# Kernel tuning notes

Hardware: AMD Instinct MI355X
Metric: run time of the kernel (lower is better)

## Reference

```python
import jax, jax.numpy as jnp
import numpy as np

N = 100000        # n_nodes (entities)
B = 1024          # batch of users
S = 32            # edge_threshold (sampled edges per node)
M = 64            # adj_matrix neighbors per node
D_IN = 64         # in_channel[0]
HID = 32          # out_channel[0] == in_channel[1]
D_OUT = 64        # out_channel[1]
K_STEP = 2
NUM_SAMPLE = 32
ITEM_LO, ITEM_HI = 0, 39999
SLOPE = 0.01      # leaky_relu default negative slope


def setup_inputs() -> dict:
    key = jax.random.key(0)
    ks = jax.random.split(key, 12)
    sc = lambda *sh: 1.0 / np.sqrt(sh[-1])
    return {
        "entity_embedding": jax.random.normal(ks[0], (N, D_IN), jnp.float32) * 0.1,
        "W1l": jax.random.normal(ks[1], (HID, D_IN), jnp.float32) * sc(HID, D_IN),
        "W1r": jax.random.normal(ks[2], (HID, D_IN), jnp.float32) * sc(HID, D_IN),
        "b1": jnp.zeros((HID,), jnp.float32),
        "W2l": jax.random.normal(ks[3], (D_OUT, HID), jnp.float32) * sc(D_OUT, HID),
        "W2r": jax.random.normal(ks[4], (D_OUT, HID), jnp.float32) * sc(D_OUT, HID),
        "b2": jnp.zeros((D_OUT,), jnp.float32),
        "disc_emb": jax.random.normal(ks[5], (N, D_OUT), jnp.float32) * 0.1,
        "users": jax.random.randint(ks[6], (B,), 0, ITEM_HI + 1, jnp.int32),
        "pos": jax.random.randint(ks[7], (B,), 0, ITEM_HI + 1, jnp.int32),
        "adj_matrix": jax.random.randint(ks[8], (N, M), 0, N, jnp.int32),
        "edge_matrix": jax.random.randint(ks[9], (N, S), 0, N, jnp.int32),
    }


def _leaky(x):
    return jnp.where(x >= 0, x, SLOPE * x)


def _sage(x, src, dst, Wl, Wr, b):
    # PyG SAGEConv: lin_l(mean_{j->i} x_j) + lin_r(x_i)
    sums = jax.ops.segment_sum(x[src], dst, num_segments=N)
    cnt = jax.ops.segment_sum(jnp.ones(src.shape, x.dtype), dst, num_segments=N)
    mean = sums / jnp.maximum(cnt, 1.0)[:, None]
    return mean @ Wl.T + b + x @ Wr.T


def _gcn(x, src, dst, W1l, W1r, b1, W2l, W2r, b2):
    h = _leaky(_sage(x, src, dst, W1l, W1r, b1))   # dropout = identity (eval)
    h = _sage(h, src, dst, W2l, W2r, b2)
    nrm = jnp.sqrt(jnp.sum(h * h, axis=1, keepdims=True))
    return h / jnp.maximum(nrm, 1e-12)             # F.normalize


def _kg_step(gcn, pos_idx, users, adj, explore_flag, step):
    u_e = gcn[users]                               # [B, d]
    pos_e = gcn[pos_idx]                           # [B, d]
    one_hop = adj[pos_idx] if explore_flag == 1 else adj[users]   # [B, M]
    i_e = gcn[one_hop]                             # [B, M, d]
    p = jnp.einsum('bmd,bd->bm', _leaky(pos_e[:, None, :] * i_e), u_e)
    logits = jax.nn.softmax(p, axis=1)
    if step == 1:
        nid = jnp.argmax(logits, axis=1)[:, None]
    else:
        _, nid = jax.lax.top_k(logits, NUM_SAMPLE)
    cand = jnp.take_along_axis(one_hop, nid, axis=1)
    prob = jnp.log(jnp.take_along_axis(logits, nid, axis=1))
    if step == 1:
        return cand[:, 0], prob[:, 0]
    return cand, prob


def _filter_entity(cand, key):
    rnd = jax.random.randint(key, cand.shape, ITEM_LO, ITEM_HI + 1, dtype=cand.dtype)
    bad = (cand > ITEM_HI) | (cand < ITEM_LO)
    return jnp.where(bad, rnd, cand)


def _prune_step(disc_emb, users, pos2, negs, logits):
    # stand-in for discriminator.item_rank (no_grad in original)
    u = jax.lax.stop_gradient(disc_emb[users])
    ranking = jnp.einsum('bd,bjd->bj', u,
                         jax.lax.stop_gradient(disc_emb[pos2] - disc_emb[negs]))
    idx = jnp.argmin(ranking, axis=1)[:, None]
    good_neg = jnp.take_along_axis(negs, idx, axis=1)[:, 0]
    good_logits = jnp.take_along_axis(logits, idx, axis=1)[:, 0]
    return good_neg, good_logits


def reference(entity_embedding, W1l, W1r, b1, W2l, W2r, b2, disc_emb,
              users, pos, adj_matrix, edge_matrix):
    src = jnp.repeat(jnp.arange(N, dtype=jnp.int32), S)   # build_edge node_index
    dst = edge_matrix.reshape(-1)
    gcn = _gcn(entity_embedding, src, dst, W1l, W1r, b1, W2l, W2r, b2)
    fkey = jax.random.key(123)
    neg_list, prob_list = [], []
    p = pos
    for k in range(K_STEP):
        one_hop, one_hop_logits = _kg_step(gcn, p, users, adj_matrix, 1, 1)
        cand, two_logits = _kg_step(gcn, one_hop, users, adj_matrix, 1, 2)
        cand = _filter_entity(cand, jax.random.fold_in(fkey, 2 * k))
        pos2, _ = _kg_step(gcn, p, users, adj_matrix, 2, 2)
        pos2 = _filter_entity(pos2, jax.random.fold_in(fkey, 2 * k + 1))
        good_neg, good_logits = _prune_step(disc_emb, users, pos2, cand, two_logits)
        good_logits = good_logits + one_hop_logits
        neg_list.append(good_neg)
        prob_list.append(good_logits)
        p = good_neg
    return jnp.stack(neg_list), jnp.stack(prob_list)
```

## Files before the change

### kernel.cpp

```cpp
#include <hip/hip_runtime.h>
#include <hip/hip_bf16.h>

#define N_NODES 100000
#define N_EDGES (N_NODES * 32)
#define BATCH   1024
#define SPAN    40000u
#define MULT    7296u
#define FILL_B  (N_EDGES / 256)

#define NB_BKT 391
#define EPB    4096
#define SBLK   782
#define BKT_CAP 8960


__host__ __device__ inline void threefry2x32(unsigned k0, unsigned k1,
                                             unsigned x0, unsigned x1,
                                             unsigned* o0, unsigned* o1)
{
  unsigned ks2 = k0 ^ k1 ^ 0x1BD11BDAu;
  unsigned v0 = x0 + k0, v1 = x1 + k1;
#define RL(x,d) (((x) << (d)) | ((x) >> (32 - (d))))
#define G4(a,b,c,dd) \
  v0 += v1; v1 = RL(v1,a);  v1 ^= v0; \
  v0 += v1; v1 = RL(v1,b);  v1 ^= v0; \
  v0 += v1; v1 = RL(v1,c);  v1 ^= v0; \
  v0 += v1; v1 = RL(v1,dd); v1 ^= v0;
  G4(13,15,26,6)  v0 += k1;  v1 += ks2 + 1u;
  G4(17,29,16,24) v0 += ks2; v1 += k0 + 2u;
  G4(13,15,26,6)  v0 += k0;  v1 += k1 + 3u;
  G4(17,29,16,24) v0 += k1;  v1 += ks2 + 4u;
  G4(13,15,26,6)  v0 += ks2; v1 += k0 + 5u;
#undef G4
#undef RL
  *o0 = v0; *o1 = v1;
}

__device__ __forceinline__ float bcastf(float v, int l)
{
  return __int_as_float(__builtin_amdgcn_readlane(__float_as_int(v), l));
}

__device__ __forceinline__ float fbar(float v)
{
  asm volatile("" : "+v"(v));
  return v;
}


__global__ void k_init_buckets(int* __restrict__ bbase, int* __restrict__ bcur)
{
  int i = blockIdx.x * 256 + threadIdx.x;
  if (i < NB_BKT) { bbase[i] = i * BKT_CAP; bcur[i] = i * BKT_CAP; }
}

__global__ __launch_bounds__(256) void k_bucket_hist(
    const int* __restrict__ edge, int* __restrict__ bhist)
{
  __shared__ int h[NB_BKT];
  for (int i = threadIdx.x; i < NB_BKT; i += 256) h[i] = 0;
  __syncthreads();
  int base = blockIdx.x * EPB;
  int cnt = N_EDGES - base; if (cnt > EPB) cnt = EPB;
  const int4* e4 = (const int4*)(edge + base);
  int nq = cnt >> 2;
  for (int i = threadIdx.x; i < nq; i += 256) {
    int4 v = e4[i];
    atomicAdd(&h[v.x >> 8], 1); atomicAdd(&h[v.y >> 8], 1);
    atomicAdd(&h[v.z >> 8], 1); atomicAdd(&h[v.w >> 8], 1);
  }
  __syncthreads();
  for (int i = threadIdx.x; i < NB_BKT; i += 256)
    if (h[i]) atomicAdd(&bhist[i], h[i]);
}

__global__ void k_scan_buckets(const int* __restrict__ bhist,
                               int* __restrict__ bbase, int* __restrict__ bcur)
{
  __shared__ int s[512];
  int t = threadIdx.x;
  s[t] = (t < NB_BKT) ? bhist[t] : 0;
  __syncthreads();
  for (int o = 1; o < 512; o <<= 1) {
    int u = (t >= o) ? s[t - o] : 0;
    __syncthreads();
    s[t] += u;
    __syncthreads();
  }
  if (t < NB_BKT) {
    int excl = s[t] - bhist[t];
    bbase[t] = excl;
    bcur[t]  = excl;
  }
}

__global__ __launch_bounds__(256) void k_bucket_scatter(
    const int* __restrict__ edge, int* __restrict__ bcur,
    int* __restrict__ pairs)
{
  __shared__ int  h[NB_BKT];
  __shared__ int  lbase[NB_BKT];
  __shared__ int  gbase[NB_BKT];
  __shared__ int  lcur[NB_BKT];
  __shared__ int2 buf[EPB];
  int t = threadIdx.x;
  for (int i = t; i < NB_BKT; i += 256) h[i] = 0;
  __syncthreads();
  int base = blockIdx.x * EPB;
  int cnt = N_EDGES - base; if (cnt > EPB) cnt = EPB;
  const int4* e4 = (const int4*)(edge + base);
  int nq = cnt >> 2;
  for (int i = t; i < nq; i += 256) {
    int4 v = e4[i];
    atomicAdd(&h[v.x >> 8], 1); atomicAdd(&h[v.y >> 8], 1);
    atomicAdd(&h[v.z >> 8], 1); atomicAdd(&h[v.w >> 8], 1);
  }
  __syncthreads();
  if (t < 64) {
    int run = 0;
    for (int c = 0; c < NB_BKT; c += 64) {
      int idx = c + t;
      int v = (idx < NB_BKT) ? h[idx] : 0;
      int orig = v;
      for (int o = 1; o < 64; o <<= 1) {
        int u = __shfl_up(v, o);
        if (t >= o) v += u;
      }
      if (idx < NB_BKT) lbase[idx] = run + v - orig;
      run += __shfl(v, 63);
    }
  }
  __syncthreads();
  for (int i = t; i < NB_BKT; i += 256) lcur[i] = lbase[i];
  __syncthreads();
  for (int i = t; i < nq; i += 256) {
    int4 v = e4[i];
    int eid = base + (i << 2);
    int p;
    p = atomicAdd(&lcur[v.x >> 8], 1); buf[p] = make_int2(v.x, (eid + 0) >> 5);
    p = atomicAdd(&lcur[v.y >> 8], 1); buf[p] = make_int2(v.y, (eid + 1) >> 5);
    p = atomicAdd(&lcur[v.z >> 8], 1); buf[p] = make_int2(v.z, (eid + 2) >> 5);
    p = atomicAdd(&lcur[v.w >> 8], 1); buf[p] = make_int2(v.w, (eid + 3) >> 5);
  }
  __syncthreads();
  for (int i = t; i < NB_BKT; i += 256) {
    int c = lcur[i] - lbase[i];
    gbase[i] = (c > 0) ? atomicAdd(&bcur[i], c) : 0;
  }
  __syncthreads();
  for (int i = t; i < cnt; i += 256) {
    int2 pr = buf[i];
    int b = pr.x >> 8;
    pairs[gbase[b] + (i - lbase[b])] = (pr.y << 8) | (pr.x & 255);
  }
}

__global__ __launch_bounds__(256) void k_bucket_csr(
    const int* __restrict__ bbase, const int* __restrict__ bcur,
    const int* __restrict__ pairs, int* __restrict__ csr,
    int* __restrict__ rowp, int* __restrict__ deg)
{
  __shared__ int nd[256], nb[256], nc[256];
  int b = blockIdx.x, t = threadIdx.x;
  int nb0 = b << 8;
  int ebase = bbase[b];
  int ecnt  = bcur[b] - ebase;
  nd[t] = 0; nc[t] = 0;
  __syncthreads();
  for (int i = t; i < ecnt; i += 256) {
    int pr = pairs[ebase + i];
    atomicAdd(&nd[pr & 255], 1);
  }
  __syncthreads();
  nb[t] = nd[t];
  __syncthreads();
  for (int o = 1; o < 256; o <<= 1) {
    int u = (t >= o) ? nb[t - o] : 0;
    __syncthreads();
    nb[t] += u;
    __syncthreads();
  }
  int excl = nb[t] - nd[t];
  int node = nb0 + t;
  if (node < N_NODES) { rowp[node] = ebase + excl; deg[node] = nd[t]; }
  __syncthreads();
  nb[t] = excl;
  __syncthreads();
  for (int i = t; i < ecnt; i += 256) {
    int pr = pairs[ebase + i];
    int l = pr & 255;
    int p = atomicAdd(&nc[l], 1);
    csr[ebase + nb[l] + p] = pr >> 8;
  }
}

__global__ __launch_bounds__(256) void k_gather_csr(
    const int* __restrict__ rowp, const int* __restrict__ deg,
    const int* __restrict__ csr, const float* __restrict__ src,
    float* __restrict__ out)
{
  int node = blockIdx.x * 8 + (threadIdx.x >> 5);
  int f = threadIdx.x & 31;
  int hb = threadIdx.x & 32;
  int sub = f >> 3;
  int q   = f & 7;
  int start = rowp[node];
  int dg = deg[node];
  const float4* src4 = (const float4*)src;
  float4 a0 = make_float4(0.f, 0.f, 0.f, 0.f);
  float4 a1 = make_float4(0.f, 0.f, 0.f, 0.f);
  for (int b0 = 0; b0 < dg; b0 += 32) {
    int idx = b0 + f;
    int e = (idx < dg) ? csr[start + idx] : -1;
#pragma unroll
    for (int j = 0; j < 8; j += 2) {
      int e0 = __shfl(e, hb + 4 * j + sub);
      int e1 = __shfl(e, hb + 4 * (j + 1) + sub);
      if (e0 >= 0) {
        float4 v = src4[(size_t)e0 * 8 + q];
        a0.x += v.x; a0.y += v.y; a0.z += v.z; a0.w += v.w;
      }
      if (e1 >= 0) {
        float4 v = src4[(size_t)e1 * 8 + q];
        a1.x += v.x; a1.y += v.y; a1.z += v.z; a1.w += v.w;
      }
    }
  }
  a0.x += a1.x; a0.y += a1.y; a0.z += a1.z; a0.w += a1.w;
  a0.x += __shfl_xor(a0.x, 8);  a0.y += __shfl_xor(a0.y, 8);
  a0.z += __shfl_xor(a0.z, 8);  a0.w += __shfl_xor(a0.w, 8);
  a0.x += __shfl_xor(a0.x, 16); a0.y += __shfl_xor(a0.y, 16);
  a0.z += __shfl_xor(a0.z, 16); a0.w += __shfl_xor(a0.w, 16);
  if (sub == 0) ((float4*)out)[(size_t)node * 8 + q] = a0;
}

__global__ __launch_bounds__(256) void k_fill_gemm(
    const int* __restrict__ edge, int* __restrict__ head, int* __restrict__ next,
    int nsub, const float* __restrict__ x, const float* __restrict__ W,
    float* __restrict__ y)
{
  __shared__ float sw[32 * 65];
  if (blockIdx.x < FILL_B) {
    int e = blockIdx.x * 256 + threadIdx.x;
    int d = edge[e];
    int sub = e & (nsub - 1);
    int old = atomicExch(head + sub * N_NODES + d, e);
    next[e] = old;
  } else {
    for (int t = threadIdx.x; t < 2048; t += 256) sw[(t >> 6) * 65 + (t & 63)] = W[t];
    __syncthreads();
    int i = (blockIdx.x - FILL_B) * 8 + (threadIdx.x >> 5);
    int f = threadIdx.x & 31;
    const float* xr = x + (size_t)i * 64;
    const float* wr = sw + f * 65;
    float acc = 0.f;
#pragma unroll
    for (int d = 0; d < 64; ++d) acc += xr[d] * wr[d];
    y[(size_t)i * 32 + f] = acc;
  }
}

template<int NSUB>
__global__ __launch_bounds__(256) void k_gather_ll(
    const int* __restrict__ head, const int* __restrict__ next,
    const float* __restrict__ src, float* __restrict__ out,
    int* __restrict__ deg_out)
{
  int node = blockIdx.x * 8 + (threadIdx.x >> 5);
  int f = threadIdx.x & 31;
  int hb = threadIdx.x & 32;
  int e = (f < NSUB) ? head[f * N_NODES + node] : -1;
  float acc = 0.f;
  int cnt = 0;
  while (true) {
    int es[NSUB];
    bool any = false;
#pragma unroll
    for (int j = 0; j < NSUB; ++j) { es[j] = __shfl(e, hb + j); any |= (es[j] != -1); }
    if (!any) break;
    int en = -1;
    if (f < NSUB && e != -1) en = next[e];
#pragma unroll
    for (int j = 0; j < NSUB; ++j)
      if (es[j] != -1) { acc += src[(size_t)(es[j] >> 5) * 32 + f]; cnt++; }
    e = en;
  }
  out[(size_t)node * 32 + f] = acc;
  if (deg_out != nullptr && f == 0) deg_out[node] = cnt;
}

#define DGB 391

__global__ __launch_bounds__(256, 4) void k_gemm64x32(
    const float* __restrict__ x, const float* __restrict__ W, float* __restrict__ y)
{
  int lane = threadIdx.x & 63;
  int wv = blockIdx.x * 4 + (threadIdx.x >> 6);
  int node = wv * 64 + lane;
  bool ok = node < N_NODES;
  const float4* x4 = (const float4*)(x + (size_t)node * 64);
  const float4* W4 = (const float4*)W;
  float acc[32];
#pragma unroll
  for (int o = 0; o < 32; ++o) acc[o] = 0.f;
#pragma unroll 1
  for (int j = 0; j < 16; ++j) {
    float4 xv = ok ? x4[j] : make_float4(0.f, 0.f, 0.f, 0.f);
#pragma unroll
    for (int o = 0; o < 32; ++o) {
      float4 wv4 = W4[o * 16 + j];
      acc[o] += wv4.x * xv.x;
      acc[o] += wv4.y * xv.y;
      acc[o] += wv4.z * xv.z;
      acc[o] += wv4.w * xv.w;
    }
  }
  if (ok) {
    float4* y4 = (float4*)(y + (size_t)node * 32);
#pragma unroll
    for (int k = 0; k < 8; ++k)
      y4[k] = make_float4(acc[4 * k], acc[4 * k + 1], acc[4 * k + 2], acc[4 * k + 3]);
  }
}

__global__ __launch_bounds__(256) void k_scatter(
    const int* __restrict__ edge, const float* __restrict__ src,
    float* __restrict__ acc, int* __restrict__ cnt)
{
  int e = blockIdx.x * 8 + (threadIdx.x >> 5);
  int f = threadIdx.x & 31;
  int d = edge[e];
  atomicAdd(acc + (size_t)d * 32 + f, src[(size_t)(e >> 5) * 32 + f]);
  if (cnt != nullptr && f == 0) atomicAdd(cnt + d, 1);
}

__global__ __launch_bounds__(256, 4) void k_layer1(
    const float* __restrict__ sum1, const int* __restrict__ cnt,
    const float* __restrict__ x, const float* __restrict__ W1r,
    const float* __restrict__ b1, float* __restrict__ h)
{
  int lane = threadIdx.x & 63;
  int wv = blockIdx.x * 4 + (threadIdx.x >> 6);
  int node = wv * 64 + lane;
  bool ok = node < N_NODES;
  const float4* x4 = (const float4*)(x + (size_t)node * 64);
  const float4* W4 = (const float4*)W1r;
  float acc[32];
#pragma unroll
  for (int o = 0; o < 32; ++o) acc[o] = 0.f;
#pragma unroll 1
  for (int j = 0; j < 16; ++j) {
    float4 xv = ok ? x4[j] : make_float4(0.f, 0.f, 0.f, 0.f);
#pragma unroll
    for (int o = 0; o < 32; ++o) {
      float4 wv4 = W4[o * 16 + j];
      acc[o] += wv4.x * xv.x;
      acc[o] += wv4.y * xv.y;
      acc[o] += wv4.z * xv.z;
      acc[o] += wv4.w * xv.w;
    }
  }
  if (ok) {
    float c = fmaxf((float)cnt[node], 1.f);
    const float4* s4 = (const float4*)(sum1 + (size_t)node * 32);
    float4* h4 = (float4*)(h + (size_t)node * 32);
#pragma unroll
    for (int k = 0; k < 8; ++k) {
      float4 sv = s4[k];
      float4 r;
      r.x = ((sv.x / c) + b1[4 * k + 0]) + acc[4 * k + 0];
      r.y = ((sv.y / c) + b1[4 * k + 1]) + acc[4 * k + 1];
      r.z = ((sv.z / c) + b1[4 * k + 2]) + acc[4 * k + 2];
      r.w = ((sv.w / c) + b1[4 * k + 3]) + acc[4 * k + 3];
      r.x = (r.x >= 0.f) ? r.x : 0.01f * r.x;
      r.y = (r.y >= 0.f) ? r.y : 0.01f * r.y;
      r.z = (r.z >= 0.f) ? r.z : 0.01f * r.z;
      r.w = (r.w >= 0.f) ? r.w : 0.01f * r.w;
      h4[k] = r;
    }
  }
}

#define L2B 782

__global__ __launch_bounds__(256, 4) void k_layer2(
    float* __restrict__ A, float* __restrict__ B, const int* __restrict__ cnt,
    const float* __restrict__ W2l, const float* __restrict__ W2r,
    const float* __restrict__ b2)
{
  int lane = threadIdx.x & 63;
  int wv = blockIdx.x * 4 + (threadIdx.x >> 6);
  int node = wv * 32 + (lane >> 1);
  int half = lane & 1;
  bool ok = node < N_NODES;
  float c = 1.f;
  if (ok) c = fmaxf((float)cnt[node], 1.f);
  const float4* B4 = (const float4*)(B + (size_t)node * 32);
  const float4* A4 = (const float4*)(A + (size_t)node * 32);
  const float4* Wl4 = (const float4*)W2l + half * 256;
  const float4* Wr4 = (const float4*)W2r + half * 256;
  const float* b2h = b2 + half * 32;

  float t[32];
#pragma unroll
  for (int o = 0; o < 32; ++o) t[o] = 0.f;
#pragma unroll 1
  for (int j = 0; j < 8; ++j) {
    float4 bv = ok ? B4[j] : make_float4(0.f, 0.f, 0.f, 0.f);
    bv.x /= c; bv.y /= c; bv.z /= c; bv.w /= c;
#pragma unroll
    for (int o = 0; o < 32; ++o) {
      float4 w = Wl4[o * 8 + j];
      t[o] += w.x * bv.x;
      t[o] += w.y * bv.y;
      t[o] += w.z * bv.z;
      t[o] += w.w * bv.w;
    }
  }
#pragma unroll
  for (int o = 0; o < 32; ++o) t[o] = t[o] + b2h[o];
  {
    float acc2[32];
#pragma unroll
    for (int o = 0; o < 32; ++o) acc2[o] = 0.f;
#pragma unroll 1
    for (int j = 0; j < 8; ++j) {
      float4 av = ok ? A4[j] : make_float4(0.f, 0.f, 0.f, 0.f);
#pragma unroll
      for (int o = 0; o < 32; ++o) {
        float4 w = Wr4[o * 8 + j];
        acc2[o] += w.x * av.x;
        acc2[o] += w.y * av.y;
        acc2[o] += w.z * av.z;
        acc2[o] += w.w * av.w;
      }
    }
#pragma unroll
    for (int o = 0; o < 32; ++o) t[o] = t[o] + acc2[o];
  }

  float a[32];
#pragma unroll
  for (int k = 0; k < 32; ++k) {
    float sq = fbar(t[k] * t[k]);
    float other = __shfl_xor(sq, 1);
    a[k] = sq + other;
  }
  float bv[16];
#pragma unroll
  for (int k = 0; k < 16; ++k) bv[k] = a[k] + a[k + 16];
  float cv[8];
#pragma unroll
  for (int k = 0; k < 8; ++k) cv[k] = bv[k] + bv[k + 8];
  float dv[4];
#pragma unroll
  for (int k = 0; k < 4; ++k) dv[k] = cv[k] + cv[k + 4];
  float ev0 = dv[0] + dv[2], ev1 = dv[1] + dv[3];
  float s = (ev0 + ev1);
  float den = fmaxf(sqrtf(s), 1e-12f);
  if (ok) {
    float* dst = (half == 0) ? (A + (size_t)node * 32) : (B + (size_t)node * 32);
    float4* D4 = (float4*)dst;
#pragma unroll
    for (int k = 0; k < 8; ++k) {
      D4[k] = make_float4(t[4 * k] / den, t[4 * k + 1] / den,
                          t[4 * k + 2] / den, t[4 * k + 3] / den);
    }
  }
}


__device__ inline float kg_score_lds(const float* __restrict__ row,
                                     const float* sp, const float* su)
{
  float acc = 0.f;
#pragma unroll
  for (int d = 0; d < 64; ++d) {
    float t = sp[d] * row[d];
    t = (t >= 0.f) ? t : 0.01f * t;
    acc += t * su[d];
  }
  return acc;
}

__device__ inline float wave_softmax(float acc)
{
  float m = acc;
#pragma unroll
  for (int o = 32; o > 0; o >>= 1) m = fmaxf(m, __shfl_xor(m, o));
  float e = expf(acc - m);
  float Z = e;
#pragma unroll
  for (int o = 32; o > 0; o >>= 1) Z += __shfl_xor(Z, o);
  return e / Z;
}

__device__ inline void load_row(const float* glo, const float* ghi, int node,
                                int lane, float* smem)
{
  smem[lane] = (lane < 32) ? glo[(size_t)node * 32 + lane]
                           : ghi[(size_t)node * 32 + (lane - 32)];
}

__device__ inline void stage_rows(const float* __restrict__ glo,
                                  const float* __restrict__ ghi,
                                  int nb, int lane, float* sn)
{
#pragma unroll
  for (int j = 0; j < 64; ++j) {
    int rj = __builtin_amdgcn_readlane(nb, j);
    float v = (lane < 32) ? glo[(size_t)rj * 32 + lane]
                          : ghi[(size_t)rj * 32 + (lane - 32)];
    sn[j * 65 + lane] = v;
  }
}

__global__ __launch_bounds__(64) void k_kg_argmax(
    const float* __restrict__ glo, const float* __restrict__ ghi,
    const int* __restrict__ users, const int* __restrict__ pvec,
    const int* __restrict__ adj, int* __restrict__ sel_out,
    float* __restrict__ logit_out)
{
  int b = blockIdx.x, lane = threadIdx.x;
  int u = users[b], pb = pvec[b];
  __shared__ float su[64], sp[64];
  __shared__ float sn[64 * 65];
  load_row(glo, ghi, u,  lane, su);
  load_row(glo, ghi, pb, lane, sp);
  int nb = adj[(size_t)pb * 64 + lane];
  stage_rows(glo, ghi, nb, lane, sn);
  __syncthreads();
  float sm = wave_softmax(kg_score_lds(sn + lane * 65, sp, su));
  float v = sm; int i = lane;
#pragma unroll
  for (int o = 32; o > 0; o >>= 1) {
    float ov = __shfl_xor(v, o); int oi = __shfl_xor(i, o);
    if (ov > v || (ov == v && oi < i)) { v = ov; i = oi; }
  }
  float smw = __shfl(sm, i);
  int sel = __shfl(nb, i);
  if (lane == 0) { sel_out[b] = sel; logit_out[b] = logf(smw); }
}

__global__ __launch_bounds__(64) void k_kg_topk2(
    const float* __restrict__ glo, const float* __restrict__ ghi,
    const int* __restrict__ users, const int* __restrict__ srcA,
    const int* __restrict__ pvecB, const int* __restrict__ adj,
    unsigned a1a, unsigned a1b, unsigned a2a, unsigned a2b,
    unsigned c1a, unsigned c1b, unsigned c2a, unsigned c2b,
    int* __restrict__ candA, float* __restrict__ logA, int* __restrict__ candB)
{
  int b = blockIdx.x & (BATCH - 1);
  int var = blockIdx.x >> 10;
  int lane = threadIdx.x;
  int u = users[b];
  int pidx = (var == 0) ? srcA[b] : pvecB[b];
  int nbr  = (var == 0) ? srcA[b] : u;
  unsigned k1a = (var == 0) ? a1a : c1a, k1b = (var == 0) ? a1b : c1b;
  unsigned k2a = (var == 0) ? a2a : c2a, k2b = (var == 0) ? a2b : c2b;
  int* cand_out = (var == 0) ? candA : candB;
  float* logit_out = (var == 0) ? logA : nullptr;

  __shared__ float su[64], sp[64];
  __shared__ float sn[64 * 65];
  load_row(glo, ghi, u,    lane, su);
  load_row(glo, ghi, pidx, lane, sp);
  int nb = adj[(size_t)nbr * 64 + lane];
  stage_rows(glo, ghi, nb, lane, sn);
  __syncthreads();
  float sm = wave_softmax(kg_score_lds(sn + lane * 65, sp, su));
  int r = 0;
#pragma unroll
  for (int j = 0; j < 64; ++j) {
    float sj = bcastf(sm, j);
    if (sj > sm || (sj == sm && j < lane)) ++r;
  }
  if (r < 32) {
    int cand = nb;
    if (logit_out != nullptr) logit_out[b * 32 + r] = logf(sm);
    unsigned j = (unsigned)(b * 32 + r);
    unsigned h0, h1, l0, l1;
    threefry2x32(k1a, k1b, 0u, j, &h0, &h1);
    threefry2x32(k2a, k2b, 0u, j, &l0, &l1);
    unsigned hi = h0 ^ h1, lo = l0 ^ l1;
    unsigned rnd = ((hi % SPAN) * MULT + (lo % SPAN)) % SPAN;
    if (cand > 39999 || cand < 0) cand = (int)rnd;
    cand_out[b * 32 + r] = cand;
  }
}

__global__ __launch_bounds__(64) void k_kg_prune(
    const float* __restrict__ disc, const int* __restrict__ users,
    const int* __restrict__ cand, const float* __restrict__ two_log,
    const int* __restrict__ pos2, const float* __restrict__ one_log,
    float* __restrict__ out, int k, int* __restrict__ p_next)
{
  int b = blockIdx.x, lane = threadIdx.x;
  __shared__ float su[64];
  __shared__ float sd[64 * 65];
  su[lane] = disc[(size_t)users[b] * 64 + lane];
  int pr = (lane < 32) ? pos2[b * 32 + lane] : cand[b * 32 + (lane - 32)];
#pragma unroll
  for (int j = 0; j < 64; ++j) {
    int rj = __builtin_amdgcn_readlane(pr, j);
    sd[j * 65 + lane] = disc[(size_t)rj * 64 + lane];
  }
  __syncthreads();
  float r = 1e30f;
  if (lane < 32) {
    const float* dp = sd + lane * 65;
    const float* dn = sd + (32 + lane) * 65;
    float acc = 0.f;
#pragma unroll
    for (int d = 0; d < 64; ++d) acc += su[d] * (dp[d] - dn[d]);
    r = acc;
  }
  float v = r; int i = lane;
#pragma unroll
  for (int o = 32; o > 0; o >>= 1) {
    float ov = __shfl_xor(v, o); int oi = __shfl_xor(i, o);
    if (ov < v || (ov == v && oi < i)) { v = ov; i = oi; }
  }
  if (lane == 0) {
    int gn = cand[b * 32 + i];
    float gl = two_log[b * 32 + i] + one_log[b];
    out[k * BATCH + b]             = (float)gn;
    out[2 * BATCH + k * BATCH + b] = gl;
    p_next[b] = gn;
  }
}

extern "C" void kernel_launch(void* const* d_in, const int* in_sizes, int n_in,
                              void* d_out, int out_size, void* d_ws, size_t ws_size,
                              hipStream_t stream)
{
  const float* x    = (const float*)d_in[0];
  const float* W1l  = (const float*)d_in[1];
  const float* W1r  = (const float*)d_in[2];
  const float* b1   = (const float*)d_in[3];
  const float* W2l  = (const float*)d_in[4];
  const float* W2r  = (const float*)d_in[5];
  const float* b2   = (const float*)d_in[6];
  const float* disc = (const float*)d_in[7];
  const int*   users= (const int*)d_in[8];
  const int*   pos  = (const int*)d_in[9];
  const int*   adj  = (const int*)d_in[10];
  const int*   edge = (const int*)d_in[11];
  float* out = (float*)d_out;

  char* w = (char*)d_ws;
  const size_t NEED_FIX = 42036480;
  const size_t NEED_CSR = 39617792;
  float *A, *B;
  char* bb;

  if (ws_size >= NEED_FIX) {
    int*  csr   = (int*)(w);
    int*  rowp  = (int*)(w + 14013440);
    int*  deg   = (int*)(w + 14413440);
    int*  bbase = (int*)(w + 14813440);
    int*  bcur  = (int*)(w + 14815488);
    int*  pairs = (int*)(w + 14817536);
    A = (float*)(w + 14817536);
    B = (float*)(w + 28830976);
    bb = w + 41630976;
    k_init_buckets<<<2, 256, 0, stream>>>(bbase, bcur);
    k_bucket_scatter<<<SBLK, 256, 0, stream>>>(edge, bcur, pairs);
    k_bucket_csr<<<NB_BKT, 256, 0, stream>>>(bbase, bcur, pairs, csr, rowp, deg);
    k_gemm64x32<<<DGB, 256, 0, stream>>>(x, W1l, A);
    k_gather_csr<<<N_NODES / 8, 256, 0, stream>>>(rowp, deg, csr, A, B);
    k_layer1<<<DGB, 256, 0, stream>>>(B, deg, x, W1r, b1, A);
    k_gather_csr<<<N_NODES / 8, 256, 0, stream>>>(rowp, deg, csr, A, B);
    k_layer2<<<L2B, 256, 0, stream>>>(A, B, deg, W2l, W2r, b2);
  } else if (ws_size >= NEED_CSR) {
    int*  csr   = (int*)(w);
    int*  rowp  = (int*)(w + 12800000);
    int*  deg   = (int*)(w + 13200000);
    int*  bhist = (int*)(w + 13600000);
    int*  bbase = (int*)(w + 13604096);
    int*  bcur  = (int*)(w + 13608192);
    int*  pairs = (int*)(w + 13612288);
    A = (float*)(w + 13612288);
    B = (float*)(w + 26412288);
    bb = w + 39212288;
    hipMemsetAsync(bhist, 0, 4096, stream);
    k_bucket_hist<<<SBLK, 256, 0, stream>>>(edge, bhist);
    k_scan_buckets<<<1, 512, 0, stream>>>(bhist, bbase, bcur);
    k_bucket_scatter<<<SBLK, 256, 0, stream>>>(edge, bcur, pairs);
    k_bucket_csr<<<NB_BKT, 256, 0, stream>>>(bbase, bcur, pairs, csr, rowp, deg);
    k_gemm64x32<<<DGB, 256, 0, stream>>>(x, W1l, A);
    k_gather_csr<<<N_NODES / 8, 256, 0, stream>>>(rowp, deg, csr, A, B);
    k_layer1<<<DGB, 256, 0, stream>>>(B, deg, x, W1r, b1, A);
    k_gather_csr<<<N_NODES / 8, 256, 0, stream>>>(rowp, deg, csr, A, B);
    k_layer2<<<L2B, 256, 0, stream>>>(A, B, deg, W2l, W2r, b2);
  } else {
    int* cnt = (int*)w;
    A = (float*)(w + 409600);
    B = (float*)(w + 13209600);
    bb = w + 26009600;
    hipMemsetAsync(cnt, 0, 400000, stream);
    hipMemsetAsync(B, 0, 12800000, stream);
    k_gemm64x32<<<DGB, 256, 0, stream>>>(x, W1l, A);
    k_scatter<<<N_EDGES / 8, 256, 0, stream>>>(edge, A, B, cnt);
    k_layer1<<<DGB, 256, 0, stream>>>(B, cnt, x, W1r, b1, A);
    hipMemsetAsync(B, 0, 12800000, stream);
    k_scatter<<<N_EDGES / 8, 256, 0, stream>>>(edge, A, B, nullptr);
    k_layer2<<<L2B, 256, 0, stream>>>(A, B, cnt, W2l, W2r, b2);
  }

  int*   p_cur       = (int*)(bb);
  int*   one_hop_sel = (int*)(bb + 4096);
  float* one_hop_log = (float*)(bb + 8192);
  int*   cand        = (int*)(bb + 12288);
  float* two_log     = (float*)(bb + 143360);
  int*   pos2        = (int*)(bb + 274432);

  for (int k = 0; k < 2; ++k) {
    unsigned f0, f1, a1a, a1b, a2a, a2b, c1a, c1b, c2a, c2b;
    threefry2x32(0u, 123u, 0u, (unsigned)(2 * k), &f0, &f1);
    threefry2x32(f0, f1, 0u, 0u, &a1a, &a1b);
    threefry2x32(f0, f1, 0u, 1u, &a2a, &a2b);
    threefry2x32(0u, 123u, 0u, (unsigned)(2 * k + 1), &f0, &f1);
    threefry2x32(f0, f1, 0u, 0u, &c1a, &c1b);
    threefry2x32(f0, f1, 0u, 1u, &c2a, &c2b);

    const int* pvec = (k == 0) ? pos : p_cur;
    k_kg_argmax<<<BATCH, 64, 0, stream>>>(A, B, users, pvec, adj, one_hop_sel, one_hop_log);
    k_kg_topk2<<<2 * BATCH, 64, 0, stream>>>(A, B, users, one_hop_sel, pvec, adj,
                                             a1a, a1b, a2a, a2b, c1a, c1b, c2a, c2b,
                                             cand, two_log, pos2);
    k_kg_prune<<<BATCH, 64, 0, stream>>>(disc, users, cand, two_log, pos2,
                                         one_hop_log, out, k, p_cur);
  }
}
```

Before: 510.9 us.

## Split layer-2 output halves across waves and combine norms via LDS

Remaps the layer-2 SAGE kernel so each wave owns one output half for 64 nodes, instead of two adjacent lanes splitting one node. Because the half index is now uniform across a wave, the W2l/W2r/b2 reads become wave-uniform and can be served as scalar or broadcast loads rather than per-lane vector loads. Partial outputs go to a padded LDS tile, and after a block barrier each wave reads both halves to compute the L2 norm. The cost is about 33 KB of LDS per block, which may limit occupancy, plus a __syncthreads and extra LDS traffic.

```diff
diff --git a/kernel.cpp b/kernel.cpp
--- a/kernel.cpp
+++ b/kernel.cpp
@@ -388,10 +388,12 @@
     const float* __restrict__ W2l, const float* __restrict__ W2r,
     const float* __restrict__ b2)
 {
+  __shared__ float tls[2][64 * 65];
   int lane = threadIdx.x & 63;
-  int wv = blockIdx.x * 4 + (threadIdx.x >> 6);
-  int node = wv * 32 + (lane >> 1);
-  int half = lane & 1;
+  int wid  = threadIdx.x >> 6;
+  int pair = wid >> 1;
+  int half = wid & 1;
+  int node = blockIdx.x * 128 + pair * 64 + lane;
   bool ok = node < N_NODES;
   float c = 1.f;
   if (ok) c = fmaxf((float)cnt[node], 1.f);
@@ -400,25 +402,30 @@
   const float4* Wl4 = (const float4*)W2l + half * 256;
   const float4* Wr4 = (const float4*)W2r + half * 256;
   const float* b2h = b2 + half * 32;
-
-  float t[32];
-#pragma unroll
-  for (int o = 0; o < 32; ++o) t[o] = 0.f;
+  float* myrow = &tls[pair][lane * 65];
+  float* myslot = myrow + half * 32;
+
+  {
+    float acc[32];
+#pragma unroll
+    for (int o = 0; o < 32; ++o) acc[o] = 0.f;
 #pragma unroll 1
-  for (int j = 0; j < 8; ++j) {
-    float4 bv = ok ? B4[j] : make_float4(0.f, 0.f, 0.f, 0.f);
-    bv.x /= c; bv.y /= c; bv.z /= c; bv.w /= c;
-#pragma unroll
-    for (int o = 0; o < 32; ++o) {
-      float4 w = Wl4[o * 8 + j];
-      t[o] += w.x * bv.x;
-      t[o] += w.y * bv.y;
-      t[o] += w.z * bv.z;
-      t[o] += w.w * bv.w;
+    for (int j = 0; j < 8; ++j) {
+      float4 bv = ok ? B4[j] : make_float4(0.f, 0.f, 0.f, 0.f);
+      bv.x /= c; bv.y /= c; bv.z /= c; bv.w /= c;
+#pragma unroll
+      for (int o = 0; o < 32; ++o) {
+        float4 w = Wl4[o * 8 + j];
+        acc[o] += w.x * bv.x;
+        acc[o] += w.y * bv.y;
+        acc[o] += w.z * bv.z;
+        acc[o] += w.w * bv.w;
+      }
     }
-  }
-#pragma unroll
-  for (int o = 0; o < 32; ++o) t[o] = t[o] + b2h[o];
+#pragma unroll
+    for (int o = 0; o < 32; ++o) myslot[o] = acc[o] + b2h[o];
+  }
+
   {
     float acc2[32];
 #pragma unroll
@@ -436,15 +443,19 @@
       }
     }
 #pragma unroll
-    for (int o = 0; o < 32; ++o) t[o] = t[o] + acc2[o];
-  }
+    for (int o = 0; o < 32; ++o) myslot[o] = myslot[o] + acc2[o];
+  }
+
+  __syncthreads();
 
   float a[32];
 #pragma unroll
   for (int k = 0; k < 32; ++k) {
-    float sq = fbar(t[k] * t[k]);
-    float other = __shfl_xor(sq, 1);
-    a[k] = sq + other;
+    float t0k = myrow[k];
+    float t1k = myrow[32 + k];
+    float v0 = fbar(t0k * t0k);
+    float v1 = fbar(t1k * t1k);
+    a[k] = v0 + v1;
   }
   float bv[16];
 #pragma unroll
@@ -463,8 +474,8 @@
     float4* D4 = (float4*)dst;
 #pragma unroll
     for (int k = 0; k < 8; ++k) {
-      D4[k] = make_float4(t[4 * k] / den, t[4 * k + 1] / den,
-                          t[4 * k + 2] / den, t[4 * k + 3] / den);
+      D4[k] = make_float4(myslot[4 * k] / den, myslot[4 * k + 1] / den,
+                          myslot[4 * k + 2] / den, myslot[4 * k + 3] / den);
     }
   }
 }
```

Result: faster. 467.3 us (-8.5%).
